# Optimization experiments

Hardware: AMD Instinct MI355X
Metric: run time of the kernel (lower is better)

The kernel has to match this reference:

```python
import jax, jax.numpy as jnp
import numpy as np

B, S, E, H = 4, 2048, 2048, 16
D = E // H  # head_dim = 128


def setup_inputs() -> dict:
    key = jax.random.key(0)
    ks = jax.random.split(key, 10)
    sc = 1.0 / np.sqrt(E)
    x = jax.random.normal(ks[0], (B, S, E), dtype=jnp.float32)
    causal_mask = jnp.tril(jnp.ones((S, S), dtype=jnp.int32))  # 1 = keep, 0 = mask
    wq = jax.random.normal(ks[1], (E, E), dtype=jnp.float32) * sc
    bq = jax.random.normal(ks[2], (E,), dtype=jnp.float32) * sc
    wk = jax.random.normal(ks[3], (E, E), dtype=jnp.float32) * sc
    bk = jax.random.normal(ks[4], (E,), dtype=jnp.float32) * sc
    wv = jax.random.normal(ks[5], (E, E), dtype=jnp.float32) * sc
    bv = jax.random.normal(ks[6], (E,), dtype=jnp.float32) * sc
    wo = jax.random.normal(ks[7], (E, E), dtype=jnp.float32) * sc
    bo = jax.random.normal(ks[8], (E,), dtype=jnp.float32) * sc
    return {"x": x, "causal_mask": causal_mask, "wq": wq, "bq": bq,
            "wk": wk, "bk": bk, "wv": wv, "bv": bv, "wo": wo, "bo": bo}


def _split_heads(t):
    # [B,S,E] -> [B,H,S,D]
    return t.reshape(B, S, H, D).transpose(0, 2, 1, 3)


def reference(x, causal_mask, wq, bq, wk, bk, wv, bv, wo, bo):
    # torch Linear: y = x @ W.T + b
    q = _split_heads(x @ wq.T + bq)
    k = _split_heads(x @ wk.T + bk)
    v = _split_heads(x @ wv.T + bv)
    scale = 1.0 / jnp.sqrt(jnp.asarray(D, dtype=x.dtype))
    dots = jnp.einsum("bhqd,bhkd->bhqk", q, k) * scale
    dots = jnp.where(causal_mask == 0, jnp.asarray(-jnp.inf, dots.dtype), dots)
    attn = jax.nn.softmax(dots, axis=-1)
    ctx = jnp.einsum("bhqk,bhkd->bhqd", attn, v)
    ctx = ctx.transpose(0, 2, 1, 3).reshape(B, S, E)  # merge heads
    return ctx @ wo.T + bo
```

## Files before the change

kernel.cpp:

```cpp
#include <hip/hip_runtime.h>
#include <hip/hip_bf16.h>

#define B_ 4
#define S_ 2048
#define E_ 2048
#define H_ 16
#define D_ 128
#define M_ (B_*S_)

typedef __attribute__((ext_vector_type(8))) short short8;
typedef __attribute__((ext_vector_type(4))) float f32x4;

__device__ __forceinline__ unsigned short f2bf(float f) {
  union { __hip_bfloat16 h; unsigned short u; } c;
  c.h = __float2bfloat16(f);
  return c.u;
}

__device__ __forceinline__ void gld_lds16(const void* g, void* l) {
  __builtin_amdgcn_global_load_lds((const __attribute__((address_space(1))) void*)g,
                                   (__attribute__((address_space(3))) void*)l, 16, 0, 0);
}

__global__ __launch_bounds__(256) void cast_bf16_kernel(const float* __restrict__ in,
                                                        unsigned short* __restrict__ out,
                                                        int n4) {
  int i = blockIdx.x * 256 + threadIdx.x;
  if (i >= n4) return;
  float4 v = ((const float4*)in)[i];
  ushort4 o;
  o.x = f2bf(v.x); o.y = f2bf(v.y); o.z = f2bf(v.z); o.w = f2bf(v.w);
  ((ushort4*)out)[i] = o;
}

template <typename OutT, bool TR = false>
__global__ __launch_bounds__(512) void gemm_bt256(const unsigned short* __restrict__ A,
                                                  const unsigned short* __restrict__ W,
                                                  const float* __restrict__ bias,
                                                  OutT* __restrict__ C,
                                                  int M, int N, int K, float oscale) {
  __shared__ unsigned short As[2 * 256 * 64];
  __shared__ unsigned short Bs[2 * 256 * 64];
  const int tid  = threadIdx.x;
  const int lane = tid & 63;
  const int wid  = tid >> 6;
  const int nwg = gridDim.x * gridDim.y;
  const int lin = blockIdx.x + gridDim.x * blockIdx.y;
  const int nl  = (lin & 7) * (nwg >> 3) + (lin >> 3);
  const int m0 = (nl / gridDim.x) * 256;
  const int n0 = (nl % gridDim.x) * 256;
  const int wr = (wid >> 2) * 128;
  const int wc = (wid & 3) * 64;
  const int lr  = lane & 15;
  const int lg  = lane >> 4;

  f32x4 acc[8][4];
#pragma unroll
  for (int i = 0; i < 8; i++)
#pragma unroll
    for (int j = 0; j < 4; j++) acc[i][j] = (f32x4){0.f, 0.f, 0.f, 0.f};

  const int rS = tid >> 3;
  const int uS = (tid & 7) ^ (rS & 7);
  const unsigned short* asrc = A + (size_t)(m0 + rS) * K + uS * 8;
  const unsigned short* bsrc = W + (size_t)(n0 + rS) * K + uS * 8;
  char* adst = (char*)As + wid * 1024;
  char* bdst = (char*)Bs + wid * 1024;

  const int swR = (lr & 7) << 4;
  const int nK = K >> 6;

#pragma unroll
  for (int i = 0; i < 4; ++i) {
    gld_lds16(asrc + (size_t)(64 * i) * K, adst + i * 8192);
    gld_lds16(bsrc + (size_t)(64 * i) * K, bdst + i * 8192);
  }

  for (int t = 0; t < nK; ++t) {
    const int bo = (t & 1) * 32768;
    __syncthreads();

    if (t + 1 < nK) {
      const int kt2 = (t + 1) * 64;
      const int nbo = bo ^ 32768;
#pragma unroll
      for (int i = 0; i < 4; ++i) {
        gld_lds16(asrc + kt2 + (size_t)(64 * i) * K, adst + nbo + i * 8192);
        gld_lds16(bsrc + kt2 + (size_t)(64 * i) * K, bdst + nbo + i * 8192);
      }
    }

    const char* AsB = (const char*)As + bo;
    const char* BsB = (const char*)Bs + bo;
#pragma unroll
    for (int kk = 0; kk < 2; kk++) {
      const int cb = ((kk * 4 + lg) << 4) ^ swR;
      short8 bf[4];
#pragma unroll
      for (int j = 0; j < 4; j++)
        bf[j] = *(const short8*)(BsB + (wc + j * 16 + lr) * 128 + cb);
#pragma unroll
      for (int mh = 0; mh < 2; mh++) {
        short8 af[4];
#pragma unroll
        for (int i = 0; i < 4; i++)
          af[i] = *(const short8*)(AsB + (wr + mh * 64 + i * 16 + lr) * 128 + cb);
        __builtin_amdgcn_s_setprio(1);
#pragma unroll
        for (int i = 0; i < 4; i++)
#pragma unroll
          for (int j = 0; j < 4; j++) {
            if constexpr (TR)
              acc[mh * 4 + i][j] = __builtin_amdgcn_mfma_f32_16x16x32_bf16(bf[j], af[i], acc[mh * 4 + i][j], 0, 0, 0);
            else
              acc[mh * 4 + i][j] = __builtin_amdgcn_mfma_f32_16x16x32_bf16(af[i], bf[j], acc[mh * 4 + i][j], 0, 0, 0);
          }
        __builtin_amdgcn_s_setprio(0);
      }
    }
  }

  if constexpr (TR) {
    const int lg4 = lg * 4;
#pragma unroll
    for (int j = 0; j < 4; j++) {
      const int gn = n0 + wc + j * 16 + lg4;
      const float4 bv4 = *(const float4*)&bias[gn];
#pragma unroll
      for (int i = 0; i < 8; i++) {
        const int gm = m0 + wr + i * 16 + lr;
#pragma unroll
        for (int r = 0; r < 4; r++) {
          const float v = (acc[i][j][r] + ((const float*)&bv4)[r]) * oscale;
          ((unsigned short*)C)[(size_t)(gn + r) * M + gm] = f2bf(v);
        }
      }
    }
  } else {
#pragma unroll
    for (int i = 0; i < 8; i++) {
      const int gm = m0 + wr + i * 16 + lg * 4;
#pragma unroll
      for (int j = 0; j < 4; j++) {
        const int gn = n0 + wc + j * 16 + lr;
        const float bv = bias[gn];
#pragma unroll
        for (int r = 0; r < 4; r++) {
          const float v = (acc[i][j][r] + bv) * oscale;
          if constexpr (sizeof(OutT) == 2)
            ((unsigned short*)C)[(size_t)(gm + r) * N + gn] = f2bf(v);
          else
            ((float*)C)[(size_t)(gm + r) * N + gn] = v;
        }
      }
    }
  }
}

__global__ __launch_bounds__(256, 4) void flash_attn(const unsigned short* __restrict__ Q,
                                                     const unsigned short* __restrict__ K,
                                                     const unsigned short* __restrict__ VT,
                                                     unsigned short* __restrict__ Ctx) {
  __shared__ unsigned short Ks[64 * 128];
  __shared__ unsigned short Vt[128 * 64];
  __shared__ unsigned short Pl[4 * 1024];

  const int tid  = threadIdx.x;
  const int lane = tid & 63;
  const int wid  = tid >> 6;
  const int lr  = lane & 15;
  const int lg  = lane >> 4;
  const int lk8 = lg * 8;
  const int lin = blockIdx.x + 16 * blockIdx.y + 256 * blockIdx.z;
  const int nl  = (lin & 7) * 128 + (lin >> 3);
  const int bxw = nl & 15;
  const int h   = (nl >> 4) & 15;
  const int b   = nl >> 8;
  const size_t base = ((size_t)b * S_) * E_ + (size_t)h * D_;
  const unsigned short* __restrict__ Kh = K + base;
  const unsigned short* __restrict__ VTh = VT + (size_t)(h * D_) * M_ + (size_t)b * S_;
  unsigned short* Plf = Pl + wid * 1024;

  const int rK = tid >> 4;
  const int cK = ((tid * 16) & 255) ^ ((rK & 7) << 4);
  const unsigned short* ksrcB = Kh + (size_t)rK * E_ + (cK >> 1);
  char* kdstB = (char*)Ks + wid * 1024;

  const int dVb = tid >> 3;
  const int cV  = tid & 7;
  const unsigned short* vsrcB = VTh + (size_t)dVb * M_ + (size_t)((cV ^ (dVb & 7)) * 8);
  char* vdstB = (char*)Vt + wid * 1024;

  const int plw0 = (lg >> 1) * 128 + lr * 8 + (lg & 1) * 4;
  const int plrd = lg * 128 + lr * 8;

#pragma unroll 1
  for (int half = 0; half < 2; ++half) {
    const int ti = half ? (31 - bxw) : bxw;
    const int qblk = ti * 64;
    const int q0w  = qblk + wid * 16;
    const int qrow = q0w + lr;

    short8 qf[4];
#pragma unroll
    for (int kk = 0; kk < 4; kk++)
      qf[kk] = *(const short8*)&Q[base + (size_t)qrow * E_ + kk * 32 + lk8];

    f32x4 o[8];
#pragma unroll
    for (int d0 = 0; d0 < 8; d0++) o[d0] = (f32x4){0.f, 0.f, 0.f, 0.f};
    float mrow = -INFINITY;
    float lsum = 0.f;

    const int nt = ti + 1;

    for (int t = 0; t < nt; ++t) {
      const int kv0 = t * 64;
      const size_t koff = (size_t)kv0 * E_;

#pragma unroll
      for (int p = 0; p < 4; ++p) {
        gld_lds16(ksrcB + koff + (size_t)(16 * p) * E_, kdstB + p * 4096);
        gld_lds16(vsrcB + (size_t)(32 * p) * M_ + kv0,  vdstB + p * 4096);
      }
      __syncthreads();

      f32x4 s[4];
#pragma unroll
      for (int c = 0; c < 4; c++) s[c] = (f32x4){0.f, 0.f, 0.f, 0.f};
      const int swK = (lr & 7) << 4;
      __builtin_amdgcn_s_setprio(1);
#pragma unroll
      for (int kk = 0; kk < 4; kk++) {
        const int cb = (kk * 64 + lg * 16) ^ swK;
#pragma unroll
        for (int c = 0; c < 4; c++) {
          const short8 kf = *(const short8*)((const char*)Ks + (c * 16 + lr) * 256 + cb);
          s[c] = __builtin_amdgcn_mfma_f32_16x16x32_bf16(kf, qf[kk], s[c], 0, 0, 0);
        }
      }
      __builtin_amdgcn_s_setprio(0);

      float v[4][4];
#pragma unroll
      for (int c = 0; c < 4; c++)
#pragma unroll
        for (int r = 0; r < 4; r++) v[c][r] = s[c][r];
      if (t == nt - 1) {
#pragma unroll
        for (int c = 0; c < 4; c++) {
          const int kvq = kv0 + c * 16 + lg * 4;
#pragma unroll
          for (int r = 0; r < 4; r++)
            if (kvq + r > qrow) v[c][r] = -INFINITY;
        }
      }

      float pm = fmaxf(fmaxf(fmaxf(v[0][0], v[0][1]), fmaxf(v[0][2], v[0][3])),
                       fmaxf(fmaxf(v[1][0], v[1][1]), fmaxf(v[1][2], v[1][3])));
      pm = fmaxf(pm, fmaxf(fmaxf(fmaxf(v[2][0], v[2][1]), fmaxf(v[2][2], v[2][3])),
                           fmaxf(fmaxf(v[3][0], v[3][1]), fmaxf(v[3][2], v[3][3]))));
      pm = fmaxf(pm, __shfl_xor(pm, 16));
      pm = fmaxf(pm, __shfl_xor(pm, 32));

      const float need = pm - mrow;
      if (!__all(need <= 8.f)) {
        const float mnew = fmaxf(mrow, pm);
        const float al = __expf(mrow - mnew);
        lsum *= al;
#pragma unroll
        for (int d0 = 0; d0 < 8; ++d0) {
          f32x4 tt = o[d0];
          tt[0] *= al; tt[1] *= al; tt[2] *= al; tt[3] *= al;
          o[d0] = tt;
        }
        mrow = mnew;
      }

      ushort4 wpk[4];
      float ps = 0.f;
#pragma unroll
      for (int c = 0; c < 4; c++) {
        const float e0 = __expf(v[c][0] - mrow);
        const float e1 = __expf(v[c][1] - mrow);
        const float e2 = __expf(v[c][2] - mrow);
        const float e3 = __expf(v[c][3] - mrow);
        wpk[c].x = f2bf(e0); wpk[c].y = f2bf(e1);
        wpk[c].z = f2bf(e2); wpk[c].w = f2bf(e3);
        ps += (e0 + e1) + (e2 + e3);
      }
      lsum += ps;

#pragma unroll
      for (int c = 0; c < 4; c++)
        *(ushort4*)&Plf[plw0 + c * 256] = wpk[c];
      asm volatile("s_waitcnt lgkmcnt(0)" ::: "memory");
      __builtin_amdgcn_sched_barrier(0);

      const short8 pb0 = *(const short8*)&Plf[plrd];
      const short8 pb1 = *(const short8*)&Plf[plrd + 512];
      const int d7 = lr & 7;
      __builtin_amdgcn_s_setprio(1);
#pragma unroll
      for (int d0 = 0; d0 < 8; ++d0) {
        const int d = d0 * 16 + lr;
        const short8 vb0 = *(const short8*)&Vt[d * 64 + ((lg ^ d7) << 3)];
        o[d0] = __builtin_amdgcn_mfma_f32_16x16x32_bf16(vb0, pb0, o[d0], 0, 0, 0);
        const short8 vb1 = *(const short8*)&Vt[d * 64 + (((4 + lg) ^ d7) << 3)];
        o[d0] = __builtin_amdgcn_mfma_f32_16x16x32_bf16(vb1, pb1, o[d0], 0, 0, 0);
      }
      __builtin_amdgcn_s_setprio(0);
      __syncthreads();
    }

    float ls = lsum;
    ls += __shfl_xor(ls, 16);
    ls += __shfl_xor(ls, 32);
    const float inv = 1.0f / ls;
    unsigned short* crow = Ctx + base + (size_t)qrow * E_ + lg * 4;
#pragma unroll
    for (int d0 = 0; d0 < 8; ++d0) {
      ushort4 st;
      st.x = f2bf(o[d0][0] * inv);
      st.y = f2bf(o[d0][1] * inv);
      st.z = f2bf(o[d0][2] * inv);
      st.w = f2bf(o[d0][3] * inv);
      *(ushort4*)&crow[d0 * 16] = st;
    }
  }
}

extern "C" void kernel_launch(void* const* d_in, const int* in_sizes, int n_in,
                              void* d_out, int out_size, void* d_ws, size_t ws_size,
                              hipStream_t stream) {
  const float* x  = (const float*)d_in[0];
  const float* wq = (const float*)d_in[2];
  const float* bq = (const float*)d_in[3];
  const float* wk = (const float*)d_in[4];
  const float* bk = (const float*)d_in[5];
  const float* wv = (const float*)d_in[6];
  const float* bv = (const float*)d_in[7];
  const float* wo = (const float*)d_in[8];
  const float* bo = (const float*)d_in[9];
  float* out = (float*)d_out;

  char* ws = (char*)d_ws;
  const size_t MB = 1024 * 1024;
  unsigned short* xb  = (unsigned short*)(ws);
  unsigned short* wqb = (unsigned short*)(ws + 32 * MB);
  unsigned short* wkb = (unsigned short*)(ws + 40 * MB);
  unsigned short* wvb = (unsigned short*)(ws + 48 * MB);
  unsigned short* wob = (unsigned short*)(ws + 56 * MB);
  unsigned short* Qb  = (unsigned short*)(ws + 64 * MB);
  unsigned short* Kb  = (unsigned short*)(ws + 96 * MB);
  unsigned short* VTb = (unsigned short*)(ws + 128 * MB);
  unsigned short* Cb  = (unsigned short*)(ws + 160 * MB);

  const int nx4 = M_ * E_ / 4;
  const int nw4 = E_ * E_ / 4;
  cast_bf16_kernel<<<nx4 / 256, 256, 0, stream>>>(x,  xb,  nx4);
  cast_bf16_kernel<<<nw4 / 256, 256, 0, stream>>>(wq, wqb, nw4);
  cast_bf16_kernel<<<nw4 / 256, 256, 0, stream>>>(wk, wkb, nw4);
  cast_bf16_kernel<<<nw4 / 256, 256, 0, stream>>>(wv, wvb, nw4);
  cast_bf16_kernel<<<nw4 / 256, 256, 0, stream>>>(wo, wob, nw4);

  const float scale = 0.08838834764831845f;
  dim3 gg(E_ / 256, M_ / 256);
  gemm_bt256<unsigned short><<<gg, 512, 0, stream>>>(xb, wqb, bq, Qb, M_, E_, E_, scale);
  gemm_bt256<unsigned short><<<gg, 512, 0, stream>>>(xb, wkb, bk, Kb, M_, E_, E_, 1.0f);
  gemm_bt256<unsigned short, true><<<gg, 512, 0, stream>>>(xb, wvb, bv, VTb, M_, E_, E_, 1.0f);

  flash_attn<<<dim3(S_ / 64 / 2, H_, B_), 256, 0, stream>>>(Qb, Kb, VTb, Cb);

  gemm_bt256<float><<<gg, 512, 0, stream>>>(Cb, wob, bo, out, M_, E_, E_, 1.0f);
}
```

Measured before the change: 420.1 us.

## Deepen GEMM pipeline to four-stage BK=32 ring with explicit vmcnt waits

Replaces the double-buffered BK=64 GEMM main loop with a 4-slot LDS ring of BK=32 tiles, prefetching three stages ahead. The LDS swizzle changes to suit the 64-byte rows, and __syncthreads is replaced with partial s_waitcnt vmcnt plus s_barrier so loads stay in flight across iterations. The aim is to hide global-to-LDS latency behind MFMA work. In exchange there are twice as many barriers per K and fewer MFMAs between syncs.

```diff
diff --git a/kernel.cpp b/kernel.cpp
--- a/kernel.cpp
+++ b/kernel.cpp
@@ -39,8 +39,8 @@
                                                   const float* __restrict__ bias,
                                                   OutT* __restrict__ C,
                                                   int M, int N, int K, float oscale) {
-  __shared__ unsigned short As[2 * 256 * 64];
-  __shared__ unsigned short Bs[2 * 256 * 64];
+  __shared__ unsigned short As[4 * 256 * 32];
+  __shared__ unsigned short Bs[4 * 256 * 32];
   const int tid  = threadIdx.x;
   const int lane = tid & 63;
   const int wid  = tid >> 6;
@@ -60,65 +60,73 @@
 #pragma unroll
     for (int j = 0; j < 4; j++) acc[i][j] = (f32x4){0.f, 0.f, 0.f, 0.f};
 
-  const int rS = tid >> 3;
-  const int uS = (tid & 7) ^ (rS & 7);
-  const unsigned short* asrc = A + (size_t)(m0 + rS) * K + uS * 8;
-  const unsigned short* bsrc = W + (size_t)(n0 + rS) * K + uS * 8;
+  const int rSt = tid >> 2;
+  const int uSt = (tid & 3) ^ ((rSt >> 1) & 3);
+  const unsigned short* asrc = A + (size_t)(m0 + rSt) * K + uSt * 8;
+  const unsigned short* bsrc = W + (size_t)(n0 + rSt) * K + uSt * 8;
   char* adst = (char*)As + wid * 1024;
   char* bdst = (char*)Bs + wid * 1024;
-
-  const int swR = (lr & 7) << 4;
-  const int nK = K >> 6;
-
-#pragma unroll
-  for (int i = 0; i < 4; ++i) {
-    gld_lds16(asrc + (size_t)(64 * i) * K, adst + i * 8192);
-    gld_lds16(bsrc + (size_t)(64 * i) * K, bdst + i * 8192);
+  const size_t rowK128 = (size_t)128 * K;
+
+  const int cbq = ((lg ^ ((lr >> 1) & 3)) << 4);
+  const int nT = K >> 5;
+
+  auto STAGE = [&](int s) {
+    const int sb = (s & 3) * 16384;
+    const size_t ko = (size_t)s << 5;
+    gld_lds16(asrc + ko,           adst + sb);
+    gld_lds16(asrc + ko + rowK128, adst + sb + 8192);
+    gld_lds16(bsrc + ko,           bdst + sb);
+    gld_lds16(bsrc + ko + rowK128, bdst + sb + 8192);
+  };
+
+  auto COMPUTE = [&](int t) {
+    const char* AsB = (const char*)As + (t & 3) * 16384;
+    const char* BsB = (const char*)Bs + (t & 3) * 16384;
+    short8 bf[4];
+#pragma unroll
+    for (int j = 0; j < 4; j++)
+      bf[j] = *(const short8*)(BsB + (wc + j * 16 + lr) * 64 + cbq);
+#pragma unroll
+    for (int mh = 0; mh < 2; mh++) {
+      short8 af[4];
+#pragma unroll
+      for (int i = 0; i < 4; i++)
+        af[i] = *(const short8*)(AsB + (wr + mh * 64 + i * 16 + lr) * 64 + cbq);
+      __builtin_amdgcn_s_setprio(1);
+#pragma unroll
+      for (int i = 0; i < 4; i++)
+#pragma unroll
+        for (int j = 0; j < 4; j++) {
+          if constexpr (TR)
+            acc[mh * 4 + i][j] = __builtin_amdgcn_mfma_f32_16x16x32_bf16(bf[j], af[i], acc[mh * 4 + i][j], 0, 0, 0);
+          else
+            acc[mh * 4 + i][j] = __builtin_amdgcn_mfma_f32_16x16x32_bf16(af[i], bf[j], acc[mh * 4 + i][j], 0, 0, 0);
+        }
+      __builtin_amdgcn_s_setprio(0);
+    }
+  };
+
+  STAGE(0); STAGE(1); STAGE(2);
+
+  for (int t = 0; t < nT - 2; ++t) {
+    asm volatile("s_waitcnt vmcnt(8)" ::: "memory");
+    __builtin_amdgcn_s_barrier();
+    asm volatile("" ::: "memory");
+    __builtin_amdgcn_sched_barrier(0);
+    if (t + 3 < nT) STAGE(t + 3);
+    COMPUTE(t);
   }
-
-  for (int t = 0; t < nK; ++t) {
-    const int bo = (t & 1) * 32768;
-    __syncthreads();
-
-    if (t + 1 < nK) {
-      const int kt2 = (t + 1) * 64;
-      const int nbo = bo ^ 32768;
-#pragma unroll
-      for (int i = 0; i < 4; ++i) {
-        gld_lds16(asrc + kt2 + (size_t)(64 * i) * K, adst + nbo + i * 8192);
-        gld_lds16(bsrc + kt2 + (size_t)(64 * i) * K, bdst + nbo + i * 8192);
-      }
-    }
-
-    const char* AsB = (const char*)As + bo;
-    const char* BsB = (const char*)Bs + bo;
-#pragma unroll
-    for (int kk = 0; kk < 2; kk++) {
-      const int cb = ((kk * 4 + lg) << 4) ^ swR;
-      short8 bf[4];
-#pragma unroll
-      for (int j = 0; j < 4; j++)
-        bf[j] = *(const short8*)(BsB + (wc + j * 16 + lr) * 128 + cb);
-#pragma unroll
-      for (int mh = 0; mh < 2; mh++) {
-        short8 af[4];
-#pragma unroll
-        for (int i = 0; i < 4; i++)
-          af[i] = *(const short8*)(AsB + (wr + mh * 64 + i * 16 + lr) * 128 + cb);
-        __builtin_amdgcn_s_setprio(1);
-#pragma unroll
-        for (int i = 0; i < 4; i++)
-#pragma unroll
-          for (int j = 0; j < 4; j++) {
-            if constexpr (TR)
-              acc[mh * 4 + i][j] = __builtin_amdgcn_mfma_f32_16x16x32_bf16(bf[j], af[i], acc[mh * 4 + i][j], 0, 0, 0);
-            else
-              acc[mh * 4 + i][j] = __builtin_amdgcn_mfma_f32_16x16x32_bf16(af[i], bf[j], acc[mh * 4 + i][j], 0, 0, 0);
-          }
-        __builtin_amdgcn_s_setprio(0);
-      }
-    }
-  }
+  asm volatile("s_waitcnt vmcnt(4)" ::: "memory");
+  __builtin_amdgcn_s_barrier();
+  asm volatile("" ::: "memory");
+  __builtin_amdgcn_sched_barrier(0);
+  COMPUTE(nT - 2);
+  asm volatile("s_waitcnt vmcnt(0)" ::: "memory");
+  __builtin_amdgcn_s_barrier();
+  asm volatile("" ::: "memory");
+  __builtin_amdgcn_sched_barrier(0);
+  COMPUTE(nT - 1);
 
   if constexpr (TR) {
     const int lg4 = lg * 4;
```

Result: slower. 468.2 us (+11.5%).
